# Optimization experiments

Hardware: AMD Instinct MI355X
Metric: run time of the kernel (lower is better)

Reference implementation:

```python
import jax, jax.numpy as jnp
import numpy as np
from jax.scipy.special import logsumexp

N, M, D = 4096, 4096, 512
MASS = 0.9
REG = 0.1
REG_KL = 0.01
ITERS = 100


def setup_inputs() -> dict:
    key = jax.random.key(0)
    k0, k1 = jax.random.split(key)
    return {
        "ft0": jax.random.normal(k0, (N, D), dtype=jnp.float32),
        "ft1": jax.random.normal(k1, (M, D), dtype=jnp.float32),
        "bin_score": jnp.float32(0.4),
    }


def reference(ft0, ft1, bin_score):
    # all rows have norm >> 1e-8 for randn inputs -> foreground masks are all True
    f0 = ft0 / jnp.linalg.norm(ft0, axis=-1, keepdims=True)
    f1 = ft1 / jnp.linalg.norm(ft1, axis=-1, keepdims=True)
    cos_sim = f0 @ f1.T                       # [N, M]
    n, m = cos_sim.shape

    # partial OT marginals with dustbin mass (get_partial_distributions)
    a = jnp.concatenate([jnp.full((n,), MASS / n, jnp.float32),
                         jnp.array([1.0 - MASS], jnp.float32)])
    b = jnp.concatenate([jnp.full((m,), MASS / m, jnp.float32),
                         jnp.array([1.0 - MASS], jnp.float32)])
    log_mu, log_nu = jnp.log(a), jnp.log(b)   # [n+1], [m+1]

    # augment score matrix with dustbin row/col (get_partial_ot_problem)
    top = jnp.concatenate([cos_sim, jnp.broadcast_to(bin_score, (n, 1))], axis=1)
    bot = jnp.broadcast_to(bin_score, (1, m + 1))
    couplings = jnp.concatenate([top, bot], axis=0)   # [n+1, m+1]

    lmba = 1.0 / REG                         # = 10.0
    phi = REG_KL / (REG_KL + 1.0 / lmba)     # = 0.01 / 0.11
    Z = lmba * couplings

    def body(carry, _):
        u, v = carry
        u = (log_mu - logsumexp(Z + v[None, :] * lmba, axis=1)) / lmba * phi
        v = (log_nu - logsumexp(Z + u[:, None] * lmba, axis=0)) / lmba * phi
        return (u, v), None

    u0 = jnp.zeros((n + 1,), jnp.float32)
    v0 = jnp.zeros((m + 1,), jnp.float32)
    (u, v), _ = jax.lax.scan(body, (u0, v0), None, length=ITERS)

    prob = jnp.exp(Z + u[:, None] * lmba + v[None, :] * lmba)
    # prob_add_bkg with all-True masks: identity placement, zero the corner
    return prob.at[-1, -1].set(0.0)
```

## Files before the change

kernel.cpp:

```cpp
#include <hip/hip_runtime.h>
#include <math.h>

#define Nn 4096
#define Mm 4096
#define Dd 512
#define NP 4097
#define NPB 4104

#define PHI 0.09090909090909091f
#define LMU_IN  (-8.4231266823771690f)
#define LMU_BIN (-2.3025850929940457f)
#define LOG_NP  8.3180489582454150f

typedef __attribute__((ext_vector_type(8))) __bf16 bf16x8;
typedef __attribute__((ext_vector_type(4))) float  f32x4;

__device__ __forceinline__ void load_lds16(const __bf16* g, __bf16* l) {
    __builtin_amdgcn_global_load_lds(
        (__attribute__((address_space(1))) void*)g,
        (__attribute__((address_space(3))) void*)l,
        16, 0, 0);
}

__device__ __forceinline__ float block_allreduce_256(float v, float* sb) {
    #pragma unroll
    for (int off = 32; off > 0; off >>= 1) v += __shfl_down(v, off, 64);
    __syncthreads();
    if ((threadIdx.x & 63) == 0) sb[threadIdx.x >> 6] = v;
    __syncthreads();
    return sb[0] + sb[1] + sb[2] + sb[3];
}

__global__ __launch_bounds__(256) void normalize_bins_kernel(
    const float* __restrict__ F0, const float* __restrict__ F1,
    const float* __restrict__ binp,
    __bf16* __restrict__ A, __bf16* __restrict__ B, _Float16* __restrict__ Ef,
    float* __restrict__ S0, float* __restrict__ TcA) {
    __shared__ float sb[4];
    const int row = blockIdx.x;
    const float* src = (row < Nn) ? (F0 + (size_t)row * Dd)
                                  : (F1 + (size_t)(row - Nn) * Dd);
    __bf16* dst = (row < Nn) ? (A + (size_t)row * Dd)
                             : (B + (size_t)(row - Nn) * Dd);
    const float2 x = ((const float2*)src)[threadIdx.x];
    const float s = block_allreduce_256(x.x * x.x + x.y * x.y, sb);
    const float rn = rsqrtf(s);
    dst[2 * threadIdx.x]     = (__bf16)(x.x * rn);
    dst[2 * threadIdx.x + 1] = (__bf16)(x.y * rn);

    if (row < 17) {
        const int j = row * 256 + threadIdx.x;
        if (j < NP) Ef[(size_t)Nn * NPB + j] = (_Float16)__expf(10.0f * binp[0]);
    } else if (row < 33) {
        const int i = (row - 17) * 256 + threadIdx.x;
        Ef[(size_t)i * NPB + Mm] = (_Float16)__expf(10.0f * binp[0]);
    } else if (row < 50) {
        const int k = (row - 33) * 256 + threadIdx.x;
        if (k < NP) S0[k] = 0.f;
    } else if (row < 67) {
        const int k = (row - 50) * 256 + threadIdx.x;
        if (k < NP) TcA[k] = 0.f;
    }
}

#define BMt 256
#define BKt 64
__global__ __launch_bounds__(512) void gemm_rowsum_kernel(
    const __bf16* __restrict__ A, const __bf16* __restrict__ B,
    _Float16* __restrict__ Ef, float* __restrict__ S0) {
    __shared__ __align__(16) __bf16 As[2][BMt * BKt];
    __shared__ __align__(16) __bf16 Bs[2][BMt * BKt];
    const int tid = threadIdx.x;
    const int l = tid & 63, wv = tid >> 6;
    const int wm = wv >> 2, wn = wv & 3;
    const int ln = l & 15, lq = l >> 4;
    const int row0 = blockIdx.y << 8, col0 = blockIdx.x << 8;

    f32x4 acc[8][4];
    #pragma unroll
    for (int i = 0; i < 8; ++i)
        #pragma unroll
        for (int j = 0; j < 4; ++j) acc[i][j] = (f32x4){0.f, 0.f, 0.f, 0.f};

    const __bf16* aSrc[4]; const __bf16* bSrc[4]; int dOff[4];
    #pragma unroll
    for (int p = 0; p < 4; ++p) {
        const int q = tid + p * 512;
        const int r = q >> 3, c = q & 7;
        const int cs = c ^ (r & 7);
        aSrc[p] = A + (size_t)(row0 + r) * Dd + cs * 8;
        bSrc[p] = B + (size_t)(col0 + r) * Dd + cs * 8;
        dOff[p] = q * 8;
    }

    auto STAGE = [&](int buf, int k0) {
        #pragma unroll
        for (int p = 0; p < 4; ++p) load_lds16(aSrc[p] + k0, &As[buf][dOff[p]]);
        #pragma unroll
        for (int p = 0; p < 4; ++p) load_lds16(bSrc[p] + k0, &Bs[buf][dOff[p]]);
    };

    auto COMPUTE = [&](int buf) {
        #pragma unroll
        for (int ks = 0; ks < 2; ++ks) {
            bf16x8 bfr[4];
            #pragma unroll
            for (int ni = 0; ni < 4; ++ni) {
                const int r = wn * 64 + ni * 16 + ln;
                const int pc = (ks * 4 + lq) ^ (ln & 7);
                bfr[ni] = *(const bf16x8*)&Bs[buf][r * BKt + pc * 8];
            }
            #pragma unroll
            for (int mi = 0; mi < 8; ++mi) {
                const int r = wm * 128 + mi * 16 + ln;
                const int pc = (ks * 4 + lq) ^ (ln & 7);
                const bf16x8 af = *(const bf16x8*)&As[buf][r * BKt + pc * 8];
                #pragma unroll
                for (int ni = 0; ni < 4; ++ni)
                    acc[mi][ni] = __builtin_amdgcn_mfma_f32_16x16x32_bf16(
                        af, bfr[ni], acc[mi][ni], 0, 0, 0);
            }
        }
    };

    STAGE(0, 0);
    __syncthreads();
    int buf = 0;
    for (int t = 0; t < (Dd / BKt) - 1; ++t) {
        STAGE(buf ^ 1, (t + 1) * BKt);
        COMPUTE(buf);
        __syncthreads();
        buf ^= 1;
    }
    COMPUTE(buf);

    #pragma unroll
    for (int mi = 0; mi < 8; ++mi) {
        #pragma unroll
        for (int r = 0; r < 4; ++r) {
            const int gi = row0 + wm * 128 + mi * 16 + lq * 4 + r;
            _Float16* bRow = Ef + (size_t)gi * NPB + col0 + wn * 64 + ln;
            float rs = 0.f;
            #pragma unroll
            for (int ni = 0; ni < 4; ++ni) {
                const float e = __expf(10.0f * acc[mi][ni][r]);
                bRow[ni * 16] = (_Float16)e;
                rs += e;
            }
            rs += __shfl_down(rs, 8, 64);
            rs += __shfl_down(rs, 4, 64);
            rs += __shfl_down(rs, 2, 64);
            rs += __shfl_down(rs, 1, 64);
            if (ln == 0) atomicAdd(&S0[gi], rs);
        }
    }
}

__global__ __launch_bounds__(256) void col_pass_kernel(
    const _Float16* __restrict__ Ef, const float* __restrict__ S0,
    const float* __restrict__ eUarr, const float* __restrict__ binp,
    float* __restrict__ Tc, const int mode) {
    __shared__ float evl[32];
    const int tid = threadIdx.x;
    const int t = blockIdx.x;
    const int sI = blockIdx.y;
    const int r0 = sI * 32;

    if (tid < 32) {
        const int r = r0 + tid;
        float ev;
        if (mode == 0) {
            const float ebin = __expf(10.0f * binp[0]);
            ev = __expf(PHI * (LMU_IN - __logf(S0[r] + ebin)));
        } else {
            ev = eUarr[r];
        }
        evl[tid] = ev;
    }
    __syncthreads();

    const int j0 = t * 512 + tid * 2;
    const unsigned short* base = (const unsigned short*)Ef;
    float s0 = 0.f, s1 = 0.f;
    #pragma unroll
    for (int k = 0; k < 32; ++k) {
        const int r = r0 + k;
        union { unsigned u; _Float16 h[2]; } e;
        e.u = *(const unsigned*)(base + (size_t)r * NPB + j0);
        const float ev = evl[k];
        s0 += (float)e.h[0] * ev;
        s1 += (float)e.h[1] * ev;
    }

    float ev4096 = 0.f;
    if (sI == 127) {
        ev4096 = (mode == 0)
               ? __expf(PHI * (LMU_BIN - (LOG_NP + 10.0f * binp[0])))
               : eUarr[Nn];
        union { unsigned u; _Float16 h[2]; } e;
        e.u = *(const unsigned*)(base + (size_t)Nn * NPB + j0);
        s0 += (float)e.h[0] * ev4096;
        s1 += (float)e.h[1] * ev4096;
    }
    atomicAdd(&Tc[j0], s0);
    atomicAdd(&Tc[j0 + 1], s1);

    if (t == 0 && tid < 64) {
        float sc = 0.f;
        if (tid < 32)
            sc = (float)Ef[(size_t)(r0 + tid) * NPB + Mm] * evl[tid];
        else if (tid == 32 && sI == 127)
            sc = (float)Ef[(size_t)Nn * NPB + Mm] * ev4096;
        #pragma unroll
        for (int off = 32; off > 0; off >>= 1) sc += __shfl_down(sc, off, 64);
        if (tid == 0) atomicAdd(&Tc[Mm], sc);
    }
}

__global__ __launch_bounds__(256) void row_pass2_kernel(
    const _Float16* __restrict__ Ef, const float* __restrict__ TcA,
    float* __restrict__ eU, float* __restrict__ TcB) {
    __shared__ float sb[4];
    __shared__ float wl[NP];
    const int tid = threadIdx.x;

    for (int j = tid; j < NP; j += 256) {
        const float lnu = (j < Mm) ? LMU_IN : LMU_BIN;
        wl[j] = __expf(PHI * (lnu - __logf(TcA[j])));
    }
    __syncthreads();

    const int i0 = blockIdx.x * 8;
    #pragma unroll 1
    for (int k = 0; k < 8; ++k) {
        const int i = i0 + k;
        if (i >= NP) break;
        const uint4* rowp = (const uint4*)(Ef + (size_t)i * NPB);
        float s = 0.f;
        #pragma unroll
        for (int c = 0; c < 2; ++c) {
            const int chunk = c * 256 + tid;
            union { uint4 u; _Float16 h[8]; } e;
            e.u = rowp[chunk];
            const float4 w0 = *(const float4*)&wl[chunk * 8];
            const float4 w1 = *(const float4*)&wl[chunk * 8 + 4];
            s += (float)e.h[0] * w0.x + (float)e.h[1] * w0.y
               + (float)e.h[2] * w0.z + (float)e.h[3] * w0.w
               + (float)e.h[4] * w1.x + (float)e.h[5] * w1.y
               + (float)e.h[6] * w1.z + (float)e.h[7] * w1.w;
        }
        if (tid == 0) s += (float)Ef[(size_t)i * NPB + Mm] * wl[Mm];
        s = block_allreduce_256(s, sb);
        if (tid == 0) {
            const float lmu = (i < Nn) ? LMU_IN : LMU_BIN;
            eU[i] = __expf(PHI * (lmu - __logf(s)));
        }
    }
    if (tid < 8 && i0 + tid < NP) TcB[i0 + tid] = 0.f;
}

__global__ __launch_bounds__(256) void finish_kernel(
    const _Float16* __restrict__ Ef, const float* __restrict__ eU,
    const float* __restrict__ TcB, float* __restrict__ out) {
    __shared__ float wl[NP];
    const int tid = threadIdx.x;
    for (int j = tid; j < NP; j += 256) {
        const float lnu = (j < Mm) ? LMU_IN : LMU_BIN;
        wl[j] = __expf(PHI * (lnu - __logf(TcB[j])));
    }
    __syncthreads();

    const int i0 = blockIdx.x * 8;
    #pragma unroll 1
    for (int k = 0; k < 8; ++k) {
        const int i = i0 + k;
        if (i >= NP) break;
        const float sU = eU[i];
        const _Float16* erow = Ef + (size_t)i * NPB;
        float* orow = out + (size_t)i * NP;
        for (int j = tid; j < NP; j += 256) {
            float v = (float)erow[j] * sU * wl[j];
            if (i == Nn && j == Mm) v = 0.f;
            orow[j] = v;
        }
    }
}


extern "C" void kernel_launch(void* const* d_in, const int* in_sizes, int n_in,
                              void* d_out, int out_size, void* d_ws, size_t ws_size,
                              hipStream_t stream) {
    const float* ft0 = (const float*)d_in[0];
    const float* ft1 = (const float*)d_in[1];
    const float* bin = (const float*)d_in[2];
    float* out = (float*)d_out;

    const size_t ABF_B = (size_t)Nn * Dd * 2;
    const size_t EBF_B = (size_t)NP * NPB * 2;
    const size_t VEC_B = 16400;
    __bf16*   Abf = (__bf16*)d_ws;
    __bf16*   Bbf = (__bf16*)((char*)d_ws + ABF_B);
    _Float16* Ef  = (_Float16*)((char*)d_ws + 2 * ABF_B);
    float*    eU  = (float*)((char*)d_ws + 2 * ABF_B + EBF_B);
    float*    S0  = (float*)((char*)d_ws + 2 * ABF_B + EBF_B + VEC_B);
    float*    TcA = (float*)((char*)d_ws + 2 * ABF_B + EBF_B + 2 * VEC_B);
    float*    TcB = (float*)((char*)d_ws + 2 * ABF_B + EBF_B + 3 * VEC_B);

    normalize_bins_kernel<<<Nn + Mm, 256, 0, stream>>>(ft0, ft1, bin,
                                                       Abf, Bbf, Ef, S0, TcA);
    gemm_rowsum_kernel<<<dim3(16, 16), 512, 0, stream>>>(Abf, Bbf, Ef, S0);
    col_pass_kernel<<<dim3(8, 128), 256, 0, stream>>>(Ef, S0, eU, bin, TcA, 0);
    row_pass2_kernel<<<513, 256, 0, stream>>>(Ef, TcA, eU, TcB);
    col_pass_kernel<<<dim3(8, 128), 256, 0, stream>>>(Ef, S0, eU, bin, TcB, 1);
    finish_kernel<<<513, 256, 0, stream>>>(Ef, eU, TcB, out);
}
```

Measured before the change: 192.1 us.

## Deepen GEMM LDS pipeline to four stages with smaller K tiles

```diff
diff --git a/kernel.cpp b/kernel.cpp
--- a/kernel.cpp
+++ b/kernel.cpp
@@ -63,13 +63,12 @@
     }
 }
 
-#define BMt 256
-#define BKt 64
+#define BKt 32
 __global__ __launch_bounds__(512) void gemm_rowsum_kernel(
     const __bf16* __restrict__ A, const __bf16* __restrict__ B,
     _Float16* __restrict__ Ef, float* __restrict__ S0) {
-    __shared__ __align__(16) __bf16 As[2][BMt * BKt];
-    __shared__ __align__(16) __bf16 Bs[2][BMt * BKt];
+    __shared__ __align__(16) __bf16 As[4][256 * BKt];
+    __shared__ __align__(16) __bf16 Bs[4][256 * BKt];
     const int tid = threadIdx.x;
     const int l = tid & 63, wv = tid >> 6;
     const int wm = wv >> 2, wn = wv & 3;
@@ -82,57 +81,69 @@
         #pragma unroll
         for (int j = 0; j < 4; ++j) acc[i][j] = (f32x4){0.f, 0.f, 0.f, 0.f};
 
-    const __bf16* aSrc[4]; const __bf16* bSrc[4]; int dOff[4];
-    #pragma unroll
-    for (int p = 0; p < 4; ++p) {
+    const __bf16* aSrc[2]; const __bf16* bSrc[2]; int dOff[2];
+    #pragma unroll
+    for (int p = 0; p < 2; ++p) {
         const int q = tid + p * 512;
-        const int r = q >> 3, c = q & 7;
-        const int cs = c ^ (r & 7);
-        aSrc[p] = A + (size_t)(row0 + r) * Dd + cs * 8;
-        bSrc[p] = B + (size_t)(col0 + r) * Dd + cs * 8;
+        const int r = q >> 2, c = q & 3;
+        const int cg = c ^ ((r ^ (r >> 2)) & 3);
+        aSrc[p] = A + (size_t)(row0 + r) * Dd + cg * 8;
+        bSrc[p] = B + (size_t)(col0 + r) * Dd + cg * 8;
         dOff[p] = q * 8;
     }
 
     auto STAGE = [&](int buf, int k0) {
         #pragma unroll
-        for (int p = 0; p < 4; ++p) load_lds16(aSrc[p] + k0, &As[buf][dOff[p]]);
-        #pragma unroll
-        for (int p = 0; p < 4; ++p) load_lds16(bSrc[p] + k0, &Bs[buf][dOff[p]]);
+        for (int p = 0; p < 2; ++p) {
+            load_lds16(aSrc[p] + k0, &As[buf][dOff[p]]);
+            load_lds16(bSrc[p] + k0, &Bs[buf][dOff[p]]);
+        }
     };
 
+    const int sw = (ln ^ (ln >> 2)) & 3;
     auto COMPUTE = [&](int buf) {
-        #pragma unroll
-        for (int ks = 0; ks < 2; ++ks) {
-            bf16x8 bfr[4];
+        bf16x8 bfr[4];
+        #pragma unroll
+        for (int ni = 0; ni < 4; ++ni) {
+            const int r = wn * 64 + ni * 16 + ln;
+            bfr[ni] = *(const bf16x8*)&Bs[buf][r * BKt + (lq ^ sw) * 8];
+        }
+        __builtin_amdgcn_s_setprio(1);
+        #pragma unroll
+        for (int mi = 0; mi < 8; ++mi) {
+            const int r = wm * 128 + mi * 16 + ln;
+            const bf16x8 af = *(const bf16x8*)&As[buf][r * BKt + (lq ^ sw) * 8];
             #pragma unroll
-            for (int ni = 0; ni < 4; ++ni) {
-                const int r = wn * 64 + ni * 16 + ln;
-                const int pc = (ks * 4 + lq) ^ (ln & 7);
-                bfr[ni] = *(const bf16x8*)&Bs[buf][r * BKt + pc * 8];
-            }
-            #pragma unroll
-            for (int mi = 0; mi < 8; ++mi) {
-                const int r = wm * 128 + mi * 16 + ln;
-                const int pc = (ks * 4 + lq) ^ (ln & 7);
-                const bf16x8 af = *(const bf16x8*)&As[buf][r * BKt + pc * 8];
-                #pragma unroll
-                for (int ni = 0; ni < 4; ++ni)
-                    acc[mi][ni] = __builtin_amdgcn_mfma_f32_16x16x32_bf16(
-                        af, bfr[ni], acc[mi][ni], 0, 0, 0);
-            }
-        }
+            for (int ni = 0; ni < 4; ++ni)
+                acc[mi][ni] = __builtin_amdgcn_mfma_f32_16x16x32_bf16(
+                    af, bfr[ni], acc[mi][ni], 0, 0, 0);
+        }
+        __builtin_amdgcn_s_setprio(0);
     };
 
-    STAGE(0, 0);
-    __syncthreads();
-    int buf = 0;
-    for (int t = 0; t < (Dd / BKt) - 1; ++t) {
-        STAGE(buf ^ 1, (t + 1) * BKt);
-        COMPUTE(buf);
-        __syncthreads();
-        buf ^= 1;
-    }
-    COMPUTE(buf);
+    #define WAITV(N) asm volatile("s_waitcnt vmcnt(" #N ")" ::: "memory")
+    #define BAR() __builtin_amdgcn_s_barrier()
+
+    STAGE(0, 0); STAGE(1, BKt); STAGE(2, 2 * BKt);
+
+    for (int it = 0; it < 3; ++it) {
+        #pragma unroll
+        for (int u = 0; u < 4; ++u) {
+            const int t = it * 4 + u;
+            STAGE((u + 3) & 3, (t + 3) * BKt);
+            WAITV(12); BAR();
+            COMPUTE(u);
+            BAR();
+        }
+    }
+    STAGE(3, 15 * BKt);
+    WAITV(12); BAR(); COMPUTE(0); BAR();
+    WAITV(8);  BAR(); COMPUTE(1); BAR();
+    WAITV(4);  BAR(); COMPUTE(2); BAR();
+    WAITV(0);  BAR(); COMPUTE(3);
+
+    #undef WAITV
+    #undef BAR
 
     #pragma unroll
     for (int mi = 0; mi < 8; ++mi) {
```

New measurement: 195.0 us. About the same (+1.5%).
